# Kernel tuning notes

Hardware: AMD Instinct MI355X
Metric: run time of the kernel (lower is better)

Reference implementation:

```python
import jax, jax.numpy as jnp
import numpy as np

# FP4 (E2M1) format constants from the source module
EXP_BITS = 2
MANT_BITS = 1
EXP_BIAS = 1          # 2**(EXP_BITS-1) - 1
FP4_MAX = 6.0         # (1 + 1/2) * 2**( (2**EXP_BITS - 1) - EXP_BIAS )
GROUP = 128           # w_group_size


def _float_to_fp4(x):
    """Encode float -> 4-bit code (sign|exp|mant) with subnormal support.
    Mirrors _float_to_fp(x, exp_bits=2, mant_bits=1, exp_bias=1)."""
    sign = (x < 0).astype(jnp.int32)
    xa = jnp.abs(x)
    zero = xa == 0
    xs = jnp.where(zero, jnp.float32(1e-8), xa)
    max_exp_field = (1 << EXP_BITS) - 1           # 3
    min_normal_exp = 1 - EXP_BIAS                 # 0
    exp_val = jnp.floor(jnp.log2(xs)).astype(jnp.int32)
    is_sub = exp_val < min_normal_exp
    exp_clamped = jnp.clip(exp_val, min_normal_exp, max_exp_field - EXP_BIAS)
    exp_unbiased = exp_clamped + EXP_BIAS
    ms = 1 << MANT_BITS                           # 2
    mant_normal = jnp.clip(
        jnp.round((xs / jnp.exp2(exp_clamped.astype(jnp.float32)) - 1.0) * ms),
        0, ms - 1).astype(jnp.int32)
    mant_sub = jnp.clip(
        jnp.round(xs / jnp.float32(2.0 ** min_normal_exp) * ms),
        0, ms - 1).astype(jnp.int32)
    exp_field = jnp.where(is_sub, 0, exp_unbiased)
    mant_field = jnp.where(is_sub, mant_sub, mant_normal)
    code = (sign << (EXP_BITS + MANT_BITS)) | (exp_field << MANT_BITS) | mant_field
    return jnp.where(zero, 0, code)


def _fp4_to_float(code):
    """Decode 4-bit code -> float32, with subnormals. Mirrors _fp_to_float."""
    zero = code == 0
    sign = ((code >> (EXP_BITS + MANT_BITS)) & 1).astype(jnp.float32)
    raw_exp = ((code >> MANT_BITS) & ((1 << EXP_BITS) - 1)).astype(jnp.float32)
    mant = (code & ((1 << MANT_BITS) - 1)).astype(jnp.float32)
    value_normal = (1.0 + mant / float(1 << MANT_BITS)) * jnp.exp2(raw_exp - EXP_BIAS)
    value_sub = mant / float(1 << MANT_BITS) * jnp.exp2(jnp.float32(1 - EXP_BIAS))
    v = jnp.where(raw_exp == 0, value_sub, value_normal)
    v = jnp.where(sign == 1, -v, v)
    return jnp.where(zero, jnp.float32(0.0), v)


def quantize_dequantize_weight(w):
    """Group-wise (group=128 along in_features) fp4 quantize-dequantize."""
    O, I = w.shape
    wg = w.reshape(O, I // GROUP, GROUP)
    scale = jnp.max(jnp.abs(wg), axis=-1, keepdims=True) / FP4_MAX
    scale = jnp.maximum(scale, jnp.float32(1e-8))
    code = _float_to_fp4(wg / scale)            # int32 codes in [0, 15]
    deq = _fp4_to_float(code) * scale
    return deq.reshape(O, I)


def setup_inputs() -> dict:
    key = jax.random.key(0)
    k1, k2, k3 = jax.random.split(key, 3)
    x = jax.random.normal(k1, (4, 2048, 4096), dtype=jnp.float32)
    weight = jax.random.normal(k2, (4096, 4096), dtype=jnp.float32) * 0.02
    bias = jax.random.normal(k3, (4096,), dtype=jnp.float32) * 0.01
    return {"x": x, "weight": weight, "bias": bias}


def reference(x, weight, bias):
    # fake-quantize weights to FP4 (E2M1) group-wise, then F.linear
    w_deq = quantize_dequantize_weight(weight)
    return jnp.einsum('bsi,oi->bso', x, w_deq) + bias
```

## Files before the change

kernel.cpp:

```cpp
#include <hip/hip_runtime.h>
#include <stdint.h>

#define M_TOT 8192
#define N_TOT 4096
#define K_TOT 4096
#define NTILE 64

typedef __attribute__((ext_vector_type(8))) short bf16x8;
typedef __attribute__((ext_vector_type(4))) float f32x4;
typedef __attribute__((ext_vector_type(2))) unsigned short u16x2;
typedef __attribute__((ext_vector_type(4))) unsigned short u16x4;

typedef const __attribute__((address_space(1))) void* gas1;
typedef __attribute__((address_space(3))) void* las3;

__device__ __forceinline__ unsigned short bf16_rne(float f) {
    union { float f; unsigned int u; } v; v.f = f;
    unsigned int u = v.u;
    return (unsigned short)((u + 0x7FFFu + ((u >> 16) & 1u)) >> 16);
}

__device__ __forceinline__ float fp4_qdq(float wv, float scale) {
    float a = fabsf(wv) / scale;
    float q;
    if      (a <= 0.25f) q = 0.0f;
    else if (a <  1.0f ) q = 0.5f;
    else if (a <= 1.25f) q = 1.0f;
    else if (a <  2.0f ) q = 1.5f;
    else if (a <= 2.5f ) q = 2.0f;
    else if (a <  4.0f ) q = 3.0f;
    else if (a <= 5.0f ) q = 4.0f;
    else                 q = 6.0f;
    float d = q * scale;
    return wv < 0.0f ? -d : d;
}

__global__ __launch_bounds__(256) void quant_w_kernel(const float* __restrict__ w,
                                                      unsigned short* __restrict__ wb) {
    int gwave = blockIdx.x * 4 + (threadIdx.x >> 6);
    int lane = threadIdx.x & 63;
    size_t base = (size_t)gwave * 128;
    float2 v = ((const float2*)(w + base))[lane];
    float mx = fmaxf(fabsf(v.x), fabsf(v.y));
    #pragma unroll
    for (int off = 32; off; off >>= 1) mx = fmaxf(mx, __shfl_xor(mx, off));
    float scale = fmaxf(mx / 6.0f, 1e-8f);
    u16x2 o;
    o.x = bf16_rne(fp4_qdq(v.x, scale));
    o.y = bf16_rne(fp4_qdq(v.y, scale));
    *(u16x2*)(wb + base + (size_t)lane * 2) = o;
}

__global__ __launch_bounds__(256) void cvt_x_kernel(const float* __restrict__ x,
                                                    unsigned short* __restrict__ xb) {
    const int total4 = (M_TOT * K_TOT) / 4;
    int stride = gridDim.x * blockDim.x;
    for (int i = blockIdx.x * blockDim.x + threadIdx.x; i < total4; i += stride) {
        float4 v = ((const float4*)x)[i];
        u16x4 o;
        o.x = bf16_rne(v.x); o.y = bf16_rne(v.y);
        o.z = bf16_rne(v.z); o.w = bf16_rne(v.w);
        ((u16x4*)xb)[i] = o;
    }
}


#define BAR()      __builtin_amdgcn_s_barrier()
#define SCHEDB()   __builtin_amdgcn_sched_barrier(0)
#define WAITLGKM() asm volatile("s_waitcnt lgkmcnt(0)" ::: "memory")
#define WAITVM6()  asm volatile("s_waitcnt vmcnt(6)" ::: "memory")
#define WAITVM0()  asm volatile("s_waitcnt vmcnt(0)" ::: "memory")

__global__ __launch_bounds__(512) void gemm_kernel(const unsigned short* __restrict__ A,
                                                   const unsigned short* __restrict__ B,
                                                   const float* __restrict__ bias,
                                                   float* __restrict__ C) {
    extern __shared__ unsigned char lds[];

    const int bid = blockIdx.x;
    const int xcd = bid & 7;
    const int idx = bid >> 3;
    const int tm = ((xcd >> 2) << 4) + (idx >> 2);
    const int tn = ((xcd & 3) << 2) + (idx & 3);
    const int m0 = tm << 8, n0 = tn << 8;

    const int t = threadIdx.x;
    const int l = t & 63;
    const int wid = t >> 6;
    const int wr = wid >> 2;
    const int wc = wid & 3;
    const int l15 = l & 15;
    const int q4 = l >> 4;

    const int r0g = t >> 2,        p0g = t & 3;
    const int r1g = (512 + t) >> 2, p1g = t & 3;
    const int s0g = (p0g - (r0g >> 1)) & 3;
    const int s1g = (p1g - (r1g >> 1)) & 3;
    const unsigned short* arow0 = A + (size_t)(m0 + r0g) * K_TOT + s0g * 8;
    const unsigned short* arow1 = A + (size_t)(m0 + r1g) * K_TOT + s1g * 8;
    const unsigned short* brow0 = B + (size_t)(n0 + r0g) * K_TOT + s0g * 8;
    const unsigned short* brow1 = B + (size_t)(n0 + r1g) * K_TOT + s1g * 8;
    const unsigned lo0 = (unsigned)t * 16u;
    const unsigned lo1 = lo0 + 8192u;

#define STAGE(ROW0, ROW1, MATOFF, KK, TT, BB) do {                                   \
      const unsigned _base = (unsigned)(BB) * 65536u + (MATOFF) + (KK) * 16384u;     \
      const int _ko = (TT) * 64 + (KK) * 32;                                         \
      __builtin_amdgcn_global_load_lds((gas1)(ROW0 + _ko), (las3)(lds + _base + lo0), 16, 0, 0); \
      __builtin_amdgcn_global_load_lds((gas1)(ROW1 + _ko), (las3)(lds + _base + lo1), 16, 0, 0); \
    } while (0)
#define STAGE_A(KK, TT, BB) STAGE(arow0, arow1, 0u, KK, TT, BB)
#define STAGE_B(KK, TT, BB) STAGE(brow0, brow1, 32768u, KK, TT, BB)

#define LOAD_A(QM, KK, BB) do {                                                      \
      _Pragma("unroll")                                                              \
      for (int i = 0; i < 4; ++i) {                                                  \
        int ra = wr * 128 + (QM) * 64 + i * 16 + l15;                                \
        unsigned pa = (unsigned)((q4 + (ra >> 1)) & 3);                              \
        af[i] = *(const bf16x8*)(lds + (unsigned)(BB) * 65536u + (KK) * 16384u       \
                                 + (unsigned)ra * 64u + pa * 16u);                   \
      } } while (0)

#define LOAD_B(KK, BB) do {                                                          \
      _Pragma("unroll")                                                              \
      for (int n = 0; n < 4; ++n) {                                                  \
        int rb = wc * 64 + n * 16 + l15;                                             \
        unsigned pb = (unsigned)((q4 + (rb >> 1)) & 3);                              \
        bg[n] = *(const bf16x8*)(lds + (unsigned)(BB) * 65536u + 32768u              \
                                 + (KK) * 16384u + (unsigned)rb * 64u + pb * 16u);   \
      } } while (0)

#define MFMA16(QM) do {                                                              \
      _Pragma("unroll")                                                              \
      for (int i = 0; i < 4; ++i)                                                    \
        _Pragma("unroll")                                                            \
        for (int n = 0; n < 4; ++n)                                                  \
          acc[(QM) * 4 + i][n] = __builtin_amdgcn_mfma_f32_16x16x32_bf16(            \
              af[i], bg[n], acc[(QM) * 4 + i][n], 0, 0, 0);                          \
    } while (0)

#define KTILE(U, BB) do {                                                            \
      const int tt1 = ((U) + 1 < NTILE) ? (U) + 1 : (U) - 1;                         \
      const int tt2 = ((U) + 2 < NTILE) ? (U) + 2 : (U);                             \
                                                             \
      LOAD_B(0, BB); LOAD_A(0, 0, BB);                                               \
      STAGE_A(1, tt1, 1 - (BB));                                                     \
      BAR(); WAITLGKM(); SCHEDB();                                                   \
      __builtin_amdgcn_s_setprio(1); MFMA16(0); __builtin_amdgcn_s_setprio(0);       \
      BAR(); SCHEDB();                                                               \
                                                             \
      LOAD_A(1, 0, BB);                                                              \
      STAGE_B(0, tt2, BB);                                                           \
      BAR(); WAITLGKM(); SCHEDB();                                                   \
      __builtin_amdgcn_s_setprio(1); MFMA16(1); __builtin_amdgcn_s_setprio(0);       \
      BAR(); SCHEDB();                                                               \
                                                             \
      LOAD_B(1, BB); LOAD_A(0, 1, BB);                                               \
      STAGE_A(0, tt2, BB);                                                           \
      BAR(); WAITLGKM(); SCHEDB();                                                   \
      __builtin_amdgcn_s_setprio(1); MFMA16(0); __builtin_amdgcn_s_setprio(0);       \
      BAR(); SCHEDB();                                                               \
                                                             \
      LOAD_A(1, 1, BB);                                                              \
      STAGE_B(1, tt2, BB);                                                           \
      BAR(); WAITLGKM(); SCHEDB();                                                   \
      __builtin_amdgcn_s_setprio(1); MFMA16(1); __builtin_amdgcn_s_setprio(0);       \
      WAITVM6(); BAR(); SCHEDB();                                                    \
    } while (0)

    f32x4 acc[8][4];
    #pragma unroll
    for (int i = 0; i < 8; ++i)
        #pragma unroll
        for (int j = 0; j < 4; ++j)
            acc[i][j] = (f32x4)0.0f;
    bf16x8 af[4], bg[4];

    STAGE_A(0, 0, 0); STAGE_B(0, 0, 0); STAGE_A(1, 0, 0); STAGE_B(1, 0, 0);
    STAGE_A(0, 1, 1); STAGE_B(0, 1, 1); STAGE_B(1, 1, 1);
    WAITVM6();
    BAR(); SCHEDB();

    #pragma unroll 1
    for (int u = 0; u < NTILE; u += 2) {
        KTILE(u, 0);
        KTILE(u + 1, 1);
    }
    WAITVM0();

    #pragma unroll
    for (int j = 0; j < 4; ++j) {
        int n = n0 + wc * 64 + j * 16 + l15;
        float bv = bias[n];
        #pragma unroll
        for (int i = 0; i < 8; ++i) {
            int mb = m0 + wr * 128 + i * 16 + (q4 << 2);
            #pragma unroll
            for (int r = 0; r < 4; ++r)
                C[(size_t)(mb + r) * N_TOT + n] = acc[i][j][r] + bv;
        }
    }
}

extern "C" void kernel_launch(void* const* d_in, const int* in_sizes, int n_in,
                              void* d_out, int out_size, void* d_ws, size_t ws_size,
                              hipStream_t stream) {
    const float* x    = (const float*)d_in[0];
    const float* w    = (const float*)d_in[1];
    const float* bias = (const float*)d_in[2];
    float* out = (float*)d_out;

    unsigned short* wb = (unsigned short*)d_ws;
    unsigned short* xb = wb + (size_t)N_TOT * K_TOT;

    quant_w_kernel<<<(N_TOT * K_TOT / 128) / 4, 256, 0, stream>>>(w, wb);
    cvt_x_kernel<<<2048, 256, 0, stream>>>(x, xb);

    hipFuncSetAttribute(reinterpret_cast<const void*>(gemm_kernel),
                        hipFuncAttributeMaxDynamicSharedMemorySize, 131072);
    gemm_kernel<<<512, 512, 131072, stream>>>(xb, wb, bias, out);
}
```

Before: 298.6 us.

## Fuse prep kernels and drop explicit LDS waits and sched barriers in GEMM loop

Merges the weight quantization and activation bf16 conversion into one launch, splitting blocks between the two jobs, which removes one kernel launch and the gap between launches. In the GEMM main loop it removes the explicit lgkmcnt(0) waits and most sched_barriers and leaves LDS-read waits to the compiler. This may let MFMAs start earlier, but it risks the compiler reordering LDS reads across the s_barrier or waiting less precisely, which could create races or stalls.

New measurement: 287.5 us. 3.7% less time.

```diff
diff --git a/kernel.cpp b/kernel.cpp
--- a/kernel.cpp
+++ b/kernel.cpp
@@ -35,39 +35,42 @@
     return wv < 0.0f ? -d : d;
 }
 
-__global__ __launch_bounds__(256) void quant_w_kernel(const float* __restrict__ w,
-                                                      unsigned short* __restrict__ wb) {
-    int gwave = blockIdx.x * 4 + (threadIdx.x >> 6);
-    int lane = threadIdx.x & 63;
-    size_t base = (size_t)gwave * 128;
-    float2 v = ((const float2*)(w + base))[lane];
-    float mx = fmaxf(fabsf(v.x), fabsf(v.y));
-    #pragma unroll
-    for (int off = 32; off; off >>= 1) mx = fmaxf(mx, __shfl_xor(mx, off));
-    float scale = fmaxf(mx / 6.0f, 1e-8f);
-    u16x2 o;
-    o.x = bf16_rne(fp4_qdq(v.x, scale));
-    o.y = bf16_rne(fp4_qdq(v.y, scale));
-    *(u16x2*)(wb + base + (size_t)lane * 2) = o;
-}
-
-__global__ __launch_bounds__(256) void cvt_x_kernel(const float* __restrict__ x,
-                                                    unsigned short* __restrict__ xb) {
-    const int total4 = (M_TOT * K_TOT) / 4;
-    int stride = gridDim.x * blockDim.x;
-    for (int i = blockIdx.x * blockDim.x + threadIdx.x; i < total4; i += stride) {
-        float4 v = ((const float4*)x)[i];
-        u16x4 o;
-        o.x = bf16_rne(v.x); o.y = bf16_rne(v.y);
-        o.z = bf16_rne(v.z); o.w = bf16_rne(v.w);
-        ((u16x4*)xb)[i] = o;
+__global__ __launch_bounds__(256) void prep_kernel(const float* __restrict__ w,
+                                                   unsigned short* __restrict__ wb,
+                                                   const float* __restrict__ x,
+                                                   unsigned short* __restrict__ xb) {
+    if (blockIdx.x < 2048) {
+        const int total4 = (M_TOT * K_TOT) / 4;
+        int stride = 2048 * 256;
+        for (int i = blockIdx.x * 256 + threadIdx.x; i < total4; i += stride) {
+            float4 v = ((const float4*)x)[i];
+            u16x4 o;
+            o.x = bf16_rne(v.x); o.y = bf16_rne(v.y);
+            o.z = bf16_rne(v.z); o.w = bf16_rne(v.w);
+            ((u16x4*)xb)[i] = o;
+        }
+    } else {
+        int wv0 = (blockIdx.x - 2048) * 4 + (threadIdx.x >> 6);
+        int lane = threadIdx.x & 63;
+        const int ngroups = (N_TOT * K_TOT) / 128;
+        for (int g = wv0; g < ngroups; g += 2048 * 4) {
+            size_t base = (size_t)g * 128;
+            float2 v = ((const float2*)(w + base))[lane];
+            float mx = fmaxf(fabsf(v.x), fabsf(v.y));
+            #pragma unroll
+            for (int off = 32; off; off >>= 1) mx = fmaxf(mx, __shfl_xor(mx, off));
+            float scale = fmaxf(mx / 6.0f, 1e-8f);
+            u16x2 o;
+            o.x = bf16_rne(fp4_qdq(v.x, scale));
+            o.y = bf16_rne(fp4_qdq(v.y, scale));
+            *(u16x2*)(wb + base + (size_t)lane * 2) = o;
+        }
     }
 }
 
 
 #define BAR()      __builtin_amdgcn_s_barrier()
 #define SCHEDB()   __builtin_amdgcn_sched_barrier(0)
-#define WAITLGKM() asm volatile("s_waitcnt lgkmcnt(0)" ::: "memory")
 #define WAITVM6()  asm volatile("s_waitcnt vmcnt(6)" ::: "memory")
 #define WAITVM0()  asm volatile("s_waitcnt vmcnt(0)" ::: "memory")
 
@@ -145,27 +148,27 @@
                                                              \
       LOAD_B(0, BB); LOAD_A(0, 0, BB);                                               \
       STAGE_A(1, tt1, 1 - (BB));                                                     \
-      BAR(); WAITLGKM(); SCHEDB();                                                   \
+      BAR();                                                                         \
       __builtin_amdgcn_s_setprio(1); MFMA16(0); __builtin_amdgcn_s_setprio(0);       \
-      BAR(); SCHEDB();                                                               \
+      BAR();                                                                         \
                                                              \
       LOAD_A(1, 0, BB);                                                              \
       STAGE_B(0, tt2, BB);                                                           \
-      BAR(); WAITLGKM(); SCHEDB();                                                   \
+      BAR();                                                                         \
       __builtin_amdgcn_s_setprio(1); MFMA16(1); __builtin_amdgcn_s_setprio(0);       \
-      BAR(); SCHEDB();                                                               \
+      BAR();                                                                         \
                                                              \
       LOAD_B(1, BB); LOAD_A(0, 1, BB);                                               \
       STAGE_A(0, tt2, BB);                                                           \
-      BAR(); WAITLGKM(); SCHEDB();                                                   \
+      BAR();                                                                         \
       __builtin_amdgcn_s_setprio(1); MFMA16(0); __builtin_amdgcn_s_setprio(0);       \
-      BAR(); SCHEDB();                                                               \
+      BAR();                                                                         \
                                                              \
       LOAD_A(1, 1, BB);                                                              \
       STAGE_B(1, tt2, BB);                                                           \
-      BAR(); WAITLGKM(); SCHEDB();                                                   \
+      BAR();                                                                         \
       __builtin_amdgcn_s_setprio(1); MFMA16(1); __builtin_amdgcn_s_setprio(0);       \
-      WAITVM6(); BAR(); SCHEDB();                                                    \
+      WAITVM6(); SCHEDB(); BAR();                                                    \
     } while (0)
 
     f32x4 acc[8][4];
@@ -178,8 +181,8 @@
 
     STAGE_A(0, 0, 0); STAGE_B(0, 0, 0); STAGE_A(1, 0, 0); STAGE_B(1, 0, 0);
     STAGE_A(0, 1, 1); STAGE_B(0, 1, 1); STAGE_B(1, 1, 1);
-    WAITVM6();
-    BAR(); SCHEDB();
+    WAITVM6(); SCHEDB();
+    BAR();
 
     #pragma unroll 1
     for (int u = 0; u < NTILE; u += 2) {
@@ -213,8 +216,7 @@
     unsigned short* wb = (unsigned short*)d_ws;
     unsigned short* xb = wb + (size_t)N_TOT * K_TOT;
 
-    quant_w_kernel<<<(N_TOT * K_TOT / 128) / 4, 256, 0, stream>>>(w, wb);
-    cvt_x_kernel<<<2048, 256, 0, stream>>>(x, xb);
+    prep_kernel<<<4096, 256, 0, stream>>>(w, wb, x, xb);
 
     hipFuncSetAttribute(reinterpret_cast<const void*>(gemm_kernel),
                         hipFuncAttributeMaxDynamicSharedMemorySize, 131072);
```
